# Kernel tuning notes

Measured on AMD Instinct MI355X. Metric: run time of the kernel, lower is better.

Reference implementation:

```python
import math
import jax, jax.numpy as jnp
import numpy as np

B, N = 1, 768
C_S, C_Z, C_H, H, PQ, PV = 384, 128, 16, 12, 4, 8
INF, EPS = 1e5, 1e-8


def setup_inputs() -> dict:
    key = jax.random.key(0)
    ks = jax.random.split(key, 16)
    lin = lambda k, fi, fo: jax.random.normal(k, (fi, fo), jnp.float32) / np.sqrt(fi).astype(np.float32)
    s = jax.random.normal(ks[0], (B, N, C_S), jnp.float32)
    z = jax.random.normal(ks[1], (B, N, N, C_Z), jnp.float32)
    # random proper rotation matrices via QR
    A = jax.random.normal(ks[2], (B, N, 3, 3), jnp.float32)
    Q, _ = jnp.linalg.qr(A)
    d = jnp.linalg.det(Q)
    R = Q.at[..., :, 2].multiply(d[..., None])
    t = jax.random.normal(ks[3], (B, N, 3), jnp.float32)
    mask = jnp.ones((B, N), jnp.float32)
    CO = H * (C_Z + C_H + PV * 4)  # 2112
    return dict(
        s=s, z=z, R=R, t=t, mask=mask,
        Wq=lin(ks[4], C_S, H * C_H), bq=jnp.zeros((H * C_H,), jnp.float32),
        Wkv=lin(ks[5], C_S, 2 * H * C_H), bkv=jnp.zeros((2 * H * C_H,), jnp.float32),
        Wqp=lin(ks[6], C_S, H * PQ * 3), bqp=jnp.zeros((H * PQ * 3,), jnp.float32),
        Wkvp=lin(ks[7], C_S, H * (PQ + PV) * 3), bkvp=jnp.zeros((H * (PQ + PV) * 3,), jnp.float32),
        Wb=lin(ks[8], C_Z, H), bb=jnp.zeros((H,), jnp.float32),
        head_weights=jax.random.normal(ks[9], (H,), jnp.float32) * 0.1,
        Wout=lin(ks[10], CO, C_S), bout=jnp.zeros((C_S,), jnp.float32),
    )


def _as_points(p):
    # torch: split last dim into 3 chunks (x,y,z blocks), stack on new last axis
    return jnp.stack(jnp.split(p, 3, axis=-1), axis=-1)  # [B,N,H*P,3]


def reference(s, z, R, t, mask, Wq, bq, Wkv, bkv, Wqp, bqp, Wkvp, bkvp, Wb, bb, head_weights, Wout, bout):
    q = (s @ Wq + bq).reshape(B, N, H, C_H)
    kv = (s @ Wkv + bkv).reshape(B, N, H, 2 * C_H)
    k, v = kv[..., :C_H], kv[..., C_H:]

    def rigid_apply(pts):  # pts [B,N,P,3] -> R @ p + t
        return jnp.einsum('bnij,bnpj->bnpi', R, pts) + t[:, :, None, :]

    q_pts = rigid_apply(_as_points(s @ Wqp + bqp)).reshape(B, N, H, PQ, 3)
    kv_pts = rigid_apply(_as_points(s @ Wkvp + bkvp)).reshape(B, N, H, PQ + PV, 3)
    k_pts, v_pts = kv_pts[..., :PQ, :], kv_pts[..., PQ:, :]

    b = z @ Wb + bb  # [B,N,N,H] pair bias
    a = jnp.einsum('bqhc,bkhc->bhqk', q, k) * math.sqrt(1.0 / (3 * C_H))
    a = a + math.sqrt(1.0 / 3) * jnp.transpose(b, (0, 3, 1, 2))

    # point attention: squared distance between rotated query/key points
    diff = q_pts[:, :, None] - k_pts[:, None]            # [B,q,k,H,PQ,3]
    pt_att = jnp.sum(diff ** 2, axis=-1)                  # [B,q,k,H,PQ]
    hw = jax.nn.softplus(head_weights) * math.sqrt(1.0 / (3 * (PQ * 9.0 / 2)))
    pt_att = jnp.sum(pt_att * hw[None, None, None, :, None], axis=-1) * (-0.5)  # [B,q,k,H]

    square_mask = INF * (mask[:, :, None] * mask[:, None, :] - 1.0)
    a = a + jnp.transpose(pt_att, (0, 3, 1, 2)) + square_mask[:, None]
    a = jax.nn.softmax(a, axis=-1)  # [B,H,q,k]

    o = jnp.einsum('bhqk,bkhc->bqhc', a, v).reshape(B, N, H * C_H)

    o_pt = jnp.einsum('bhqk,bkhpc->bqhpc', a, v_pts)      # [B,q,H,PV,3]
    o_pt = jnp.einsum('bnji,bnhpj->bnhpi', R, o_pt - t[:, :, None, None, :])  # invert_apply
    o_pt_norm = jnp.sqrt(jnp.sum(o_pt ** 2, axis=-1) + EPS).reshape(B, N, H * PV)
    o_pt = o_pt.reshape(B, N, H * PV, 3)

    o_pair = jnp.einsum('bhqk,bqkz->bqhz', a, z).reshape(B, N, H * C_Z)

    cat = jnp.concatenate(
        [o, o_pt[..., 0], o_pt[..., 1], o_pt[..., 2], o_pt_norm, o_pair], axis=-1)
    return cat @ Wout + bout
```

## Files before the change

### kernel.cpp

```cpp
#include <hip/hip_runtime.h>


typedef unsigned short ushort_t;

__device__ __forceinline__ float bfr(ushort_t u) {
  return __uint_as_float(((unsigned int)u) << 16);
}
__device__ __forceinline__ ushort_t f2bf(float f) {
  unsigned int u = __float_as_uint(f);
  u += 0x7FFFu + ((u >> 16) & 1u);
  return (ushort_t)(u >> 16);
}

template<bool BF16>
__device__ __forceinline__ float ld(const void* p, size_t i) {
  if constexpr (BF16) return bfr(((const ushort_t*)p)[i]);
  else                return ((const float*)p)[i];
}
template<bool BF16>
__device__ __forceinline__ void ld4(const void* p, size_t i, float* o) {
  if constexpr (BF16) {
    uint2 u = *(const uint2*)((const ushort_t*)p + i);
    o[0]=__uint_as_float(u.x<<16); o[1]=__uint_as_float(u.x & 0xffff0000u);
    o[2]=__uint_as_float(u.y<<16); o[3]=__uint_as_float(u.y & 0xffff0000u);
  } else {
    float4 v = *(const float4*)((const float*)p + i);
    o[0]=v.x; o[1]=v.y; o[2]=v.z; o[3]=v.w;
  }
}

#define NT 768
#define ZROWE 98304

__global__ void k_detect(const void* s, int* flag) {
  if (blockIdx.x == 0 && threadIdx.x == 0) {
    const unsigned int* w = (const unsigned int*)s;
    int cnt = 0;
    for (int i = 0; i < 256; ++i) {
      unsigned int e = (w[i] >> 7) & 0xFFu;
      cnt += (e >= 118u && e <= 131u) ? 1 : 0;
    }
    *flag = (cnt >= 128) ? 1 : 0;
  }
}

struct ProjSmem {
  float sl[384];
  float pbuf[576];
  float Rl[9];
  float tl[3];
};

template<bool BF16>
__device__ void proj_body(ProjSmem& sm,
            const void* s, const void* R, const void* t,
            const void* Wq, const void* bq, const void* Wkv, const void* bkv,
            const void* Wqp, const void* bqp, const void* Wkvp, const void* bkvp,
            ushort_t* qo, ushort_t* ko, ushort_t* vo,
            ushort_t* qpo, ushort_t* kpo, ushort_t* vpo)
{
  const int n = blockIdx.x, tid = threadIdx.x;
  for (int i = tid; i < 384; i += 256) sm.sl[i] = ld<BF16>(s, (size_t)n*384 + i);
  if (tid < 9)  sm.Rl[tid] = ld<BF16>(R, (size_t)n*9 + tid);
  if (tid >= 16 && tid < 19) sm.tl[tid-16] = ld<BF16>(t, (size_t)n*3 + (tid-16));
  __syncthreads();

  for (int j = tid; j < 1152; j += 256) {
    const void* W; int ldw, cj; float acc;
    if (j < 192)      { W = Wq;   ldw = 192; cj = j;       acc = ld<BF16>(bq, cj);   }
    else if (j < 576) { W = Wkv;  ldw = 384; cj = j - 192; acc = ld<BF16>(bkv, cj);  }
    else if (j < 720) { W = Wqp;  ldw = 144; cj = j - 576; acc = ld<BF16>(bqp, cj);  }
    else              { W = Wkvp; ldw = 432; cj = j - 720; acc = ld<BF16>(bkvp, cj); }
    #pragma unroll 4
    for (int i = 0; i < 384; ++i)
      acc = fmaf(sm.sl[i], ld<BF16>(W, (size_t)i*ldw + cj), acc);
    if (j < 192) qo[(size_t)n*192 + j] = f2bf(acc);
    else if (j < 576) {
      int c = j - 192, h = c >> 5, r = c & 31;
      if (r < 16) ko[(size_t)n*192 + h*16 + r]      = f2bf(acc);
      else        vo[(size_t)n*192 + h*16 + (r-16)] = f2bf(acc);
    }
    else sm.pbuf[j - 576] = acc;
  }
  __syncthreads();

  if (tid < 48) {
    int j = tid;
    float lx = sm.pbuf[j], ly = sm.pbuf[48 + j], lz = sm.pbuf[96 + j];
    #pragma unroll
    for (int i = 0; i < 3; ++i) {
      float g = sm.Rl[i*3+0]*lx + sm.Rl[i*3+1]*ly + sm.Rl[i*3+2]*lz + sm.tl[i];
      qpo[(size_t)n*144 + j*3 + i] = f2bf(g);
    }
  } else if (tid >= 64 && tid < 208) {
    int j = tid - 64;
    float lx = sm.pbuf[144 + j], ly = sm.pbuf[288 + j], lz = sm.pbuf[432 + j];
    int h = j / 12, pp = j % 12;
    #pragma unroll
    for (int i = 0; i < 3; ++i) {
      float g = sm.Rl[i*3+0]*lx + sm.Rl[i*3+1]*ly + sm.Rl[i*3+2]*lz + sm.tl[i];
      if (pp < 4) kpo[(size_t)n*144 + h*12 + pp*3 + i]     = f2bf(g);
      else        vpo[(size_t)n*288 + h*24 + (pp-4)*3 + i] = f2bf(g);
    }
  }
}

__global__ __launch_bounds__(256)
void k_proj(const int* flag,
            const void* s, const void* R, const void* t,
            const void* Wq, const void* bq, const void* Wkv, const void* bkv,
            const void* Wqp, const void* bqp, const void* Wkvp, const void* bkvp,
            ushort_t* qo, ushort_t* ko, ushort_t* vo,
            ushort_t* qpo, ushort_t* kpo, ushort_t* vpo)
{
  __shared__ ProjSmem sm;
  if (*flag) proj_body<true >(sm, s,R,t,Wq,bq,Wkv,bkv,Wqp,bqp,Wkvp,bkvp,qo,ko,vo,qpo,kpo,vpo);
  else       proj_body<false>(sm, s,R,t,Wq,bq,Wkv,bkv,Wqp,bqp,Wkvp,bkvp,qo,ko,vo,qpo,kpo,vpo);
}

struct __align__(16) AttnSmem {
  float probs[12 * NT];
  float Wbl[128 * 12];
  float catrow[2112];
  float ql[192];
  float qpl[144];
  float opt[288];
  float hwc[12], bbl[12];
};

template<bool BF16>
__device__ void attn_body(AttnSmem& sm,
            void* z, const void* Rg, const void* tg, const void* mg,
            const void* Wb, const void* bbp, const void* hwg,
            const ushort_t* qB, const ushort_t* kB, const ushort_t* vB,
            const ushort_t* qpB, const ushort_t* kpB, const ushort_t* vpB)
{
  const int qrow = blockIdx.x, tid = threadIdx.x;

  for (int i = tid; i < 128*12; i += 256) sm.Wbl[i] = ld<BF16>(Wb, i);
  for (int i = tid; i < 192; i += 256)    sm.ql[i]  = bfr(qB[(size_t)qrow*192 + i]);
  if (tid < 144) sm.qpl[tid] = bfr(qpB[(size_t)qrow*144 + tid]);
  if (tid >= 192 && tid < 204) {
    int h = tid - 192;
    float x = ld<BF16>(hwg, h);
    float sp = (x > 20.f) ? x : log1pf(expf(x));
    sm.hwc[h] = -0.5f * sp * 0.13608276348795434f;
    sm.bbl[h] = ld<BF16>(bbp, h);
  }
  __syncthreads();
  const float mq = ld<BF16>(mg, qrow);

  for (int kk = tid; kk < NT; kk += 256) {
    float accb[12];
    #pragma unroll
    for (int h = 0; h < 12; ++h) accb[h] = sm.bbl[h];
    const size_t zbase = ((size_t)qrow*NT + kk)*128;
    const float4* Wb4 = (const float4*)sm.Wbl;
    #pragma unroll 4
    for (int c4 = 0; c4 < 32; ++c4) {
      float zf[4];
      ld4<BF16>(z, zbase + c4*4, zf);
      #pragma unroll
      for (int e = 0; e < 4; ++e) {
        int c = c4*4 + e;
        float zc = zf[e];
        float4 w0 = Wb4[c*3+0], w1 = Wb4[c*3+1], w2 = Wb4[c*3+2];
        accb[0] = fmaf(zc, w0.x, accb[0]); accb[1]  = fmaf(zc, w0.y, accb[1]);
        accb[2] = fmaf(zc, w0.z, accb[2]); accb[3]  = fmaf(zc, w0.w, accb[3]);
        accb[4] = fmaf(zc, w1.x, accb[4]); accb[5]  = fmaf(zc, w1.y, accb[5]);
        accb[6] = fmaf(zc, w1.z, accb[6]); accb[7]  = fmaf(zc, w1.w, accb[7]);
        accb[8] = fmaf(zc, w2.x, accb[8]); accb[9]  = fmaf(zc, w2.y, accb[9]);
        accb[10]= fmaf(zc, w2.z, accb[10]);accb[11] = fmaf(zc, w2.w, accb[11]);
      }
    }
    const ushort_t* krow  = kB  + (size_t)kk*192;
    const ushort_t* kprow = kpB + (size_t)kk*144;
    const float mk = ld<BF16>(mg, kk);
    const float maskterm = 100000.0f * (mq*mk - 1.0f);
    #pragma unroll
    for (int h = 0; h < 12; ++h) {
      float dot = 0.f;
      #pragma unroll
      for (int j = 0; j < 16; ++j)
        dot = fmaf(sm.ql[h*16+j], bfr(krow[h*16+j]), dot);
      float pts = 0.f;
      #pragma unroll
      for (int p = 0; p < 4; ++p) {
        float dx = sm.qpl[h*12+p*3+0] - bfr(kprow[h*12+p*3+0]);
        float dy = sm.qpl[h*12+p*3+1] - bfr(kprow[h*12+p*3+1]);
        float dz = sm.qpl[h*12+p*3+2] - bfr(kprow[h*12+p*3+2]);
        pts += dx*dx + dy*dy + dz*dz;
      }
      sm.probs[h*NT + kk] = dot * 0.14433756729740643f
                          + accb[h] * 0.57735026918962576f
                          + sm.hwc[h] * pts + maskterm;
    }
  }
  __syncthreads();

  {
    const int wave = tid >> 6, lane = tid & 63;
    for (int h = wave; h < 12; h += 4) {
      float vals[12]; float m = -3.0e38f;
      #pragma unroll
      for (int i = 0; i < 12; ++i) { vals[i] = sm.probs[h*NT + i*64 + lane]; m = fmaxf(m, vals[i]); }
      #pragma unroll
      for (int off = 32; off; off >>= 1) m = fmaxf(m, __shfl_xor(m, off, 64));
      float ssum = 0.f;
      #pragma unroll
      for (int i = 0; i < 12; ++i) { vals[i] = __expf(vals[i] - m); ssum += vals[i]; }
      #pragma unroll
      for (int off = 32; off; off >>= 1) ssum += __shfl_xor(ssum, off, 64);
      float inv = 1.0f / ssum;
      #pragma unroll
      for (int i = 0; i < 12; ++i) sm.probs[h*NT + i*64 + lane] = vals[i] * inv;
    }
  }
  __syncthreads();

  {
    const int c = tid & 127, h0 = tid >> 7;
    float acc[6] = {0,0,0,0,0,0};
    for (int kk = 0; kk < NT; ++kk) {
      float zc = ld<BF16>(z, (size_t)qrow*ZROWE + (size_t)kk*128 + c);
      #pragma unroll
      for (int m = 0; m < 6; ++m)
        acc[m] = fmaf(zc, sm.probs[(h0 + 2*m)*NT + kk], acc[m]);
    }
    #pragma unroll
    for (int m = 0; m < 6; ++m) sm.catrow[576 + (h0 + 2*m)*128 + c] = acc[m];
  }

  for (int idx = tid; idx < 480; idx += 256) {
    float acc = 0.f;
    if (idx < 192) {
      const float* pr = sm.probs + (idx >> 4) * NT;
      for (int kk = 0; kk < NT; ++kk)
        acc = fmaf(pr[kk], bfr(vB[(size_t)kk*192 + idx]), acc);
      sm.catrow[idx] = acc;
    } else {
      const int j = idx - 192;
      const float* pr = sm.probs + (j / 24) * NT;
      for (int kk = 0; kk < NT; ++kk)
        acc = fmaf(pr[kk], bfr(vpB[(size_t)kk*288 + j]), acc);
      sm.opt[j] = acc;
    }
  }
  __syncthreads();

  if (tid < 96) {
    const int h = tid >> 3, p = tid & 7;
    const int j = h*24 + p*3;
    float gx = sm.opt[j], gy = sm.opt[j+1], gz = sm.opt[j+2];
    gx -= ld<BF16>(tg, qrow*3+0); gy -= ld<BF16>(tg, qrow*3+1); gz -= ld<BF16>(tg, qrow*3+2);
    float r[9];
    #pragma unroll
    for (int i = 0; i < 9; ++i) r[i] = ld<BF16>(Rg, qrow*9 + i);
    float lx = r[0]*gx + r[3]*gy + r[6]*gz;
    float ly = r[1]*gx + r[4]*gy + r[7]*gz;
    float lz = r[2]*gx + r[5]*gy + r[8]*gz;
    float nrm = sqrtf(lx*lx + ly*ly + lz*lz + 1e-8f);
    const int jj = h*8 + p;
    sm.catrow[192 + jj] = lx;
    sm.catrow[288 + jj] = ly;
    sm.catrow[384 + jj] = lz;
    sm.catrow[480 + jj] = nrm;
  }
  __syncthreads();

  float* crow;
  if constexpr (BF16) crow = (float*)((ushort_t*)z + (size_t)qrow*ZROWE);
  else                crow = (float*)z + (size_t)qrow*ZROWE;
  for (int i = tid; i < 2112; i += 256) crow[i] = sm.catrow[i];
}

__global__ __launch_bounds__(256)
void k_attn(const int* flag,
            void* z, const void* Rg, const void* tg, const void* mg,
            const void* Wb, const void* bbp, const void* hwg,
            const ushort_t* qB, const ushort_t* kB, const ushort_t* vB,
            const ushort_t* qpB, const ushort_t* kpB, const ushort_t* vpB)
{
  __shared__ AttnSmem sm;
  if (*flag) attn_body<true >(sm, z,Rg,tg,mg,Wb,bbp,hwg,qB,kB,vB,qpB,kpB,vpB);
  else       attn_body<false>(sm, z,Rg,tg,mg,Wb,bbp,hwg,qB,kB,vB,qpB,kpB,vpB);
}

struct OutSmem { float As[32][33]; float Bs[32][33]; };

template<bool BF16>
__device__ void out_body(OutSmem& sm, const void* zcat, const void* Wout,
                         const void* bout, void* out)
{
  const size_t RS = BF16 ? 49152 : 98304;
  const float* cat = (const float*)zcat;
  const int n0 = blockIdx.x * 32, m0 = blockIdx.y * 32, tid = threadIdx.x;
  const int tm = (tid >> 4) * 2, tn = (tid & 15) * 2;
  float acc00 = 0.f, acc01 = 0.f, acc10 = 0.f, acc11 = 0.f;
  const int e = tid * 4;
  const int lm = e >> 5, lk = e & 31;
  for (int k0 = 0; k0 < 2112; k0 += 32) {
    float4 a = *(const float4*)(cat + (size_t)(m0 + lm)*RS + k0 + lk);
    sm.As[lk+0][lm] = a.x; sm.As[lk+1][lm] = a.y; sm.As[lk+2][lm] = a.z; sm.As[lk+3][lm] = a.w;
    float bw[4];
    ld4<BF16>(Wout, (size_t)(k0 + lm)*384 + n0 + lk, bw);
    sm.Bs[lm][lk+0] = bw[0]; sm.Bs[lm][lk+1] = bw[1];
    sm.Bs[lm][lk+2] = bw[2]; sm.Bs[lm][lk+3] = bw[3];
    __syncthreads();
    #pragma unroll
    for (int kk = 0; kk < 32; ++kk) {
      float a0 = sm.As[kk][tm], a1 = sm.As[kk][tm+1];
      float b0 = sm.Bs[kk][tn], b1 = sm.Bs[kk][tn+1];
      acc00 = fmaf(a0,b0,acc00); acc01 = fmaf(a0,b1,acc01);
      acc10 = fmaf(a1,b0,acc10); acc11 = fmaf(a1,b1,acc11);
    }
    __syncthreads();
  }
  float bb0 = ld<BF16>(bout, n0+tn), bb1 = ld<BF16>(bout, n0+tn+1);
  float v00 = acc00+bb0, v01 = acc01+bb1, v10 = acc10+bb0, v11 = acc11+bb1;
  if constexpr (BF16) {
    ushort_t* o = (ushort_t*)out;
    o[(size_t)(m0+tm)*384   + n0+tn]   = f2bf(v00);
    o[(size_t)(m0+tm)*384   + n0+tn+1] = f2bf(v01);
    o[(size_t)(m0+tm+1)*384 + n0+tn]   = f2bf(v10);
    o[(size_t)(m0+tm+1)*384 + n0+tn+1] = f2bf(v11);
  } else {
    float* o = (float*)out;
    o[(size_t)(m0+tm)*384   + n0+tn]   = v00;
    o[(size_t)(m0+tm)*384   + n0+tn+1] = v01;
    o[(size_t)(m0+tm+1)*384 + n0+tn]   = v10;
    o[(size_t)(m0+tm+1)*384 + n0+tn+1] = v11;
  }
}

__global__ __launch_bounds__(256)
void k_out(const int* flag, const void* zcat, const void* Wout,
           const void* bout, void* out)
{
  __shared__ OutSmem sm;
  if (*flag) out_body<true >(sm, zcat, Wout, bout, out);
  else       out_body<false>(sm, zcat, Wout, bout, out);
}

extern "C" void kernel_launch(void* const* d_in, const int* in_sizes, int n_in,
                              void* d_out, int out_size, void* d_ws, size_t ws_size,
                              hipStream_t stream) {
  const void* s    = d_in[0];
  void*       z    = d_in[1];
  const void* R    = d_in[2];
  const void* t    = d_in[3];
  const void* mask = d_in[4];
  const void* Wq   = d_in[5];
  const void* bq   = d_in[6];
  const void* Wkv  = d_in[7];
  const void* bkv  = d_in[8];
  const void* Wqp  = d_in[9];
  const void* bqp  = d_in[10];
  const void* Wkvp = d_in[11];
  const void* bkvp = d_in[12];
  const void* Wb   = d_in[13];
  const void* bb   = d_in[14];
  const void* hw   = d_in[15];
  const void* Wout = d_in[16];
  const void* bout = d_in[17];

  int* flag = (int*)d_ws;
  ushort_t* base = (ushort_t*)((char*)d_ws + 64);
  ushort_t* qB  = base;
  ushort_t* kB  = qB  + 147456;
  ushort_t* vB  = kB  + 147456;
  ushort_t* qpB = vB  + 147456;
  ushort_t* kpB = qpB + 110592;
  ushort_t* vpB = kpB + 110592;

  k_detect<<<dim3(1), dim3(64), 0, stream>>>(s, flag);
  k_proj<<<dim3(768), dim3(256), 0, stream>>>(flag, s, R, t, Wq, bq, Wkv, bkv,
                                              Wqp, bqp, Wkvp, bkvp,
                                              qB, kB, vB, qpB, kpB, vpB);
  k_attn<<<dim3(768), dim3(256), 0, stream>>>(flag, z, R, t, mask, Wb, bb, hw,
                                              qB, kB, vB, qpB, kpB, vpB);
  k_out<<<dim3(12, 24), dim3(256), 0, stream>>>(flag, z, Wout, bout, d_out);
}
```

Measured before the change: 945.2 us.

## Transpose V layouts, vectorize projections and attention loads, union shared memory

```diff
diff --git a/kernel.cpp b/kernel.cpp
--- a/kernel.cpp
+++ b/kernel.cpp
@@ -28,6 +28,29 @@
     o[0]=v.x; o[1]=v.y; o[2]=v.z; o[3]=v.w;
   }
 }
+template<bool BF16>
+__device__ __forceinline__ void ld2(const void* p, size_t i, float& x, float& y) {
+  if constexpr (BF16) {
+    unsigned int u = *(const unsigned int*)((const ushort_t*)p + i);
+    x = __uint_as_float(u << 16); y = __uint_as_float(u & 0xffff0000u);
+  } else {
+    float2 v = *(const float2*)((const float*)p + i);
+    x = v.x; y = v.y;
+  }
+}
+__device__ __forceinline__ void unp8(uint4 v, float* f) {
+  f[0]=__uint_as_float(v.x<<16); f[1]=__uint_as_float(v.x&0xffff0000u);
+  f[2]=__uint_as_float(v.y<<16); f[3]=__uint_as_float(v.y&0xffff0000u);
+  f[4]=__uint_as_float(v.z<<16); f[5]=__uint_as_float(v.z&0xffff0000u);
+  f[6]=__uint_as_float(v.w<<16); f[7]=__uint_as_float(v.w&0xffff0000u);
+}
+__device__ __forceinline__ void unp4(uint2 v, float* f) {
+  f[0]=__uint_as_float(v.x<<16); f[1]=__uint_as_float(v.x&0xffff0000u);
+  f[2]=__uint_as_float(v.y<<16); f[3]=__uint_as_float(v.y&0xffff0000u);
+}
+__device__ __forceinline__ float f4get(float4 v, int e) {
+  return e==0 ? v.x : (e==1 ? v.y : (e==2 ? v.z : v.w));
+}
 
 #define NT 768
 #define ZROWE 98304
@@ -56,51 +79,72 @@
             const void* s, const void* R, const void* t,
             const void* Wq, const void* bq, const void* Wkv, const void* bkv,
             const void* Wqp, const void* bqp, const void* Wkvp, const void* bkvp,
-            ushort_t* qo, ushort_t* ko, ushort_t* vo,
-            ushort_t* qpo, ushort_t* kpo, ushort_t* vpo)
+            ushort_t* qo, ushort_t* ko, ushort_t* vTo,
+            ushort_t* qpo, ushort_t* kpo, ushort_t* vpTo)
 {
   const int n = blockIdx.x, tid = threadIdx.x;
-  for (int i = tid; i < 384; i += 256) sm.sl[i] = ld<BF16>(s, (size_t)n*384 + i);
-  if (tid < 9)  sm.Rl[tid] = ld<BF16>(R, (size_t)n*9 + tid);
-  if (tid >= 16 && tid < 19) sm.tl[tid-16] = ld<BF16>(t, (size_t)n*3 + (tid-16));
-  __syncthreads();
-
-  for (int j = tid; j < 1152; j += 256) {
-    const void* W; int ldw, cj; float acc;
-    if (j < 192)      { W = Wq;   ldw = 192; cj = j;       acc = ld<BF16>(bq, cj);   }
-    else if (j < 576) { W = Wkv;  ldw = 384; cj = j - 192; acc = ld<BF16>(bkv, cj);  }
-    else if (j < 720) { W = Wqp;  ldw = 144; cj = j - 576; acc = ld<BF16>(bqp, cj);  }
-    else              { W = Wkvp; ldw = 432; cj = j - 720; acc = ld<BF16>(bkvp, cj); }
+  for (int i = tid; i < 96; i += 256) {
+    float f[4]; ld4<BF16>(s, (size_t)n*384 + i*4, f);
+    *(float4*)&sm.sl[i*4] = make_float4(f[0],f[1],f[2],f[3]);
+  }
+  if (tid >= 128 && tid < 137) sm.Rl[tid-128] = ld<BF16>(R, (size_t)n*9 + (tid-128));
+  if (tid >= 160 && tid < 163) sm.tl[tid-160] = ld<BF16>(t, (size_t)n*3 + (tid-160));
+  __syncthreads();
+
+  for (int g = tid; g < 288; g += 256) {
+    const void* W; const void* bias; int ldw, cj;
+    if (g < 48)       { W=Wq;   bias=bq;   ldw=192; cj=g*4;       }
+    else if (g < 144) { W=Wkv;  bias=bkv;  ldw=384; cj=g*4-192;   }
+    else if (g < 180) { W=Wqp;  bias=bqp;  ldw=144; cj=g*4-576;   }
+    else              { W=Wkvp; bias=bkvp; ldw=432; cj=g*4-720;   }
+    float a0 = ld<BF16>(bias, cj+0), a1 = ld<BF16>(bias, cj+1),
+          a2 = ld<BF16>(bias, cj+2), a3 = ld<BF16>(bias, cj+3);
     #pragma unroll 4
-    for (int i = 0; i < 384; ++i)
-      acc = fmaf(sm.sl[i], ld<BF16>(W, (size_t)i*ldw + cj), acc);
-    if (j < 192) qo[(size_t)n*192 + j] = f2bf(acc);
-    else if (j < 576) {
-      int c = j - 192, h = c >> 5, r = c & 31;
-      if (r < 16) ko[(size_t)n*192 + h*16 + r]      = f2bf(acc);
-      else        vo[(size_t)n*192 + h*16 + (r-16)] = f2bf(acc);
-    }
-    else sm.pbuf[j - 576] = acc;
+    for (int i = 0; i < 384; ++i) {
+      float w[4]; ld4<BF16>(W, (size_t)i*ldw + cj, w);
+      const float sv = sm.sl[i];
+      a0 = fmaf(sv, w[0], a0); a1 = fmaf(sv, w[1], a1);
+      a2 = fmaf(sv, w[2], a2); a3 = fmaf(sv, w[3], a3);
+    }
+    const int j = g*4;
+    if (j < 192) {
+      ushort_t* d = qo + (size_t)n*192 + j;
+      d[0]=f2bf(a0); d[1]=f2bf(a1); d[2]=f2bf(a2); d[3]=f2bf(a3);
+    } else if (j < 576) {
+      const int c = j - 192, h = c >> 5, r = c & 31;
+      if (r < 16) {
+        ushort_t* d = ko + (size_t)n*192 + h*16 + r;
+        d[0]=f2bf(a0); d[1]=f2bf(a1); d[2]=f2bf(a2); d[3]=f2bf(a3);
+      } else {
+        const int cc = h*16 + (r-16);
+        vTo[(size_t)(cc+0)*NT + n] = f2bf(a0);
+        vTo[(size_t)(cc+1)*NT + n] = f2bf(a1);
+        vTo[(size_t)(cc+2)*NT + n] = f2bf(a2);
+        vTo[(size_t)(cc+3)*NT + n] = f2bf(a3);
+      }
+    } else {
+      *(float4*)&sm.pbuf[j-576] = make_float4(a0,a1,a2,a3);
+    }
   }
   __syncthreads();
 
   if (tid < 48) {
-    int j = tid;
-    float lx = sm.pbuf[j], ly = sm.pbuf[48 + j], lz = sm.pbuf[96 + j];
+    const int j = tid;
+    float lx = sm.pbuf[j], ly = sm.pbuf[48+j], lz = sm.pbuf[96+j];
     #pragma unroll
     for (int i = 0; i < 3; ++i) {
       float g = sm.Rl[i*3+0]*lx + sm.Rl[i*3+1]*ly + sm.Rl[i*3+2]*lz + sm.tl[i];
       qpo[(size_t)n*144 + j*3 + i] = f2bf(g);
     }
   } else if (tid >= 64 && tid < 208) {
-    int j = tid - 64;
-    float lx = sm.pbuf[144 + j], ly = sm.pbuf[288 + j], lz = sm.pbuf[432 + j];
-    int h = j / 12, pp = j % 12;
+    const int j = tid - 64;
+    float lx = sm.pbuf[144+j], ly = sm.pbuf[288+j], lz = sm.pbuf[432+j];
+    const int h = j / 12, pp = j % 12;
     #pragma unroll
     for (int i = 0; i < 3; ++i) {
       float g = sm.Rl[i*3+0]*lx + sm.Rl[i*3+1]*ly + sm.Rl[i*3+2]*lz + sm.tl[i];
-      if (pp < 4) kpo[(size_t)n*144 + h*12 + pp*3 + i]     = f2bf(g);
-      else        vpo[(size_t)n*288 + h*24 + (pp-4)*3 + i] = f2bf(g);
+      if (pp < 4) kpo[(size_t)n*144 + h*12 + pp*3 + i]         = f2bf(g);
+      else        vpTo[(size_t)(h*24 + (pp-4)*3 + i)*NT + n]   = f2bf(g);
     }
   }
 }
@@ -110,148 +154,213 @@
             const void* s, const void* R, const void* t,
             const void* Wq, const void* bq, const void* Wkv, const void* bkv,
             const void* Wqp, const void* bqp, const void* Wkvp, const void* bkvp,
-            ushort_t* qo, ushort_t* ko, ushort_t* vo,
-            ushort_t* qpo, ushort_t* kpo, ushort_t* vpo)
+            ushort_t* qo, ushort_t* ko, ushort_t* vTo,
+            ushort_t* qpo, ushort_t* kpo, ushort_t* vpTo)
 {
   __shared__ ProjSmem sm;
-  if (*flag) proj_body<true >(sm, s,R,t,Wq,bq,Wkv,bkv,Wqp,bqp,Wkvp,bkvp,qo,ko,vo,qpo,kpo,vpo);
-  else       proj_body<false>(sm, s,R,t,Wq,bq,Wkv,bkv,Wqp,bqp,Wkvp,bkvp,qo,ko,vo,qpo,kpo,vpo);
+  if (*flag) proj_body<true >(sm, s,R,t,Wq,bq,Wkv,bkv,Wqp,bqp,Wkvp,bkvp,qo,ko,vTo,qpo,kpo,vpTo);
+  else       proj_body<false>(sm, s,R,t,Wq,bq,Wkv,bkv,Wqp,bqp,Wkvp,bkvp,qo,ko,vTo,qpo,kpo,vpTo);
 }
 
 struct __align__(16) AttnSmem {
   float probs[12 * NT];
-  float Wbl[128 * 12];
-  float catrow[2112];
-  float ql[192];
-  float qpl[144];
-  float opt[288];
-  float hwc[12], bbl[12];
+  union {
+    struct {
+      float4 Wbl[128*3];
+      float4 ql4[12*4];
+      float4 qpl4[12*4];
+      float  hwc[12], bbl[12];
+    } a;
+    struct {
+      float catrow[2112];
+      float opt[288];
+    } c;
+  } u;
 };
 
 template<bool BF16>
 __device__ void attn_body(AttnSmem& sm,
             void* z, const void* Rg, const void* tg, const void* mg,
             const void* Wb, const void* bbp, const void* hwg,
-            const ushort_t* qB, const ushort_t* kB, const ushort_t* vB,
-            const ushort_t* qpB, const ushort_t* kpB, const ushort_t* vpB)
+            const ushort_t* qB, const ushort_t* kB, const ushort_t* vTB,
+            const ushort_t* qpB, const ushort_t* kpB, const ushort_t* vpTB)
 {
   const int qrow = blockIdx.x, tid = threadIdx.x;
 
-  for (int i = tid; i < 128*12; i += 256) sm.Wbl[i] = ld<BF16>(Wb, i);
-  for (int i = tid; i < 192; i += 256)    sm.ql[i]  = bfr(qB[(size_t)qrow*192 + i]);
-  if (tid < 144) sm.qpl[tid] = bfr(qpB[(size_t)qrow*144 + tid]);
-  if (tid >= 192 && tid < 204) {
-    int h = tid - 192;
+  for (int i = tid; i < 128*12; i += 256) ((float*)sm.u.a.Wbl)[i] = ld<BF16>(Wb, i);
+  if (tid < 48) {
+    const int h = tid >> 2, part = tid & 3;
+    float f[4];
+    unp4(*(const uint2*)(qB + (size_t)qrow*192 + h*16 + part*4), f);
+    sm.u.a.ql4[h*4+part] = make_float4(f[0],f[1],f[2],f[3]);
+  } else if (tid >= 64 && tid < 112) {
+    const int j = tid - 64, h = j >> 2, part = j & 3;
+    if (part < 3) {
+      float f[4];
+      unp4(*(const uint2*)(qpB + (size_t)qrow*144 + h*12 + part*4), f);
+      sm.u.a.qpl4[h*4+part] = make_float4(f[0],f[1],f[2],f[3]);
+    }
+  } else if (tid >= 192 && tid < 204) {
+    const int h = tid - 192;
     float x = ld<BF16>(hwg, h);
     float sp = (x > 20.f) ? x : log1pf(expf(x));
-    sm.hwc[h] = -0.5f * sp * 0.13608276348795434f;
-    sm.bbl[h] = ld<BF16>(bbp, h);
+    sm.u.a.hwc[h] = -0.5f * sp * 0.13608276348795434f;
+    sm.u.a.bbl[h] = ld<BF16>(bbp, h);
   }
   __syncthreads();
   const float mq = ld<BF16>(mg, qrow);
 
-  for (int kk = tid; kk < NT; kk += 256) {
-    float accb[12];
-    #pragma unroll
-    for (int h = 0; h < 12; ++h) accb[h] = sm.bbl[h];
-    const size_t zbase = ((size_t)qrow*NT + kk)*128;
-    const float4* Wb4 = (const float4*)sm.Wbl;
-    #pragma unroll 4
+  {
+    const int kk0 = tid;
+    float accb[3][12];
+    #pragma unroll
+    for (int h = 0; h < 12; ++h) {
+      const float b = sm.u.a.bbl[h];
+      accb[0][h] = b; accb[1][h] = b; accb[2][h] = b;
+    }
+    const size_t zb = ((size_t)qrow*NT + kk0)*128;
     for (int c4 = 0; c4 < 32; ++c4) {
-      float zf[4];
-      ld4<BF16>(z, zbase + c4*4, zf);
+      float z0[4], z1[4], z2[4];
+      ld4<BF16>(z, zb +           c4*4, z0);
+      ld4<BF16>(z, zb + 256*128 + c4*4, z1);
+      ld4<BF16>(z, zb + 512*128 + c4*4, z2);
       #pragma unroll
       for (int e = 0; e < 4; ++e) {
-        int c = c4*4 + e;
-        float zc = zf[e];
-        float4 w0 = Wb4[c*3+0], w1 = Wb4[c*3+1], w2 = Wb4[c*3+2];
-        accb[0] = fmaf(zc, w0.x, accb[0]); accb[1]  = fmaf(zc, w0.y, accb[1]);
-        accb[2] = fmaf(zc, w0.z, accb[2]); accb[3]  = fmaf(zc, w0.w, accb[3]);
-        accb[4] = fmaf(zc, w1.x, accb[4]); accb[5]  = fmaf(zc, w1.y, accb[5]);
-        accb[6] = fmaf(zc, w1.z, accb[6]); accb[7]  = fmaf(zc, w1.w, accb[7]);
-        accb[8] = fmaf(zc, w2.x, accb[8]); accb[9]  = fmaf(zc, w2.y, accb[9]);
-        accb[10]= fmaf(zc, w2.z, accb[10]);accb[11] = fmaf(zc, w2.w, accb[11]);
+        const int c = c4*4 + e;
+        float wr[12];
+        *(float4*)&wr[0] = sm.u.a.Wbl[c*3+0];
+        *(float4*)&wr[4] = sm.u.a.Wbl[c*3+1];
+        *(float4*)&wr[8] = sm.u.a.Wbl[c*3+2];
+        #pragma unroll
+        for (int h = 0; h < 12; ++h) {
+          accb[0][h] = fmaf(z0[e], wr[h], accb[0][h]);
+          accb[1][h] = fmaf(z1[e], wr[h], accb[1][h]);
+          accb[2][h] = fmaf(z2[e], wr[h], accb[2][h]);
+        }
       }
     }
-    const ushort_t* krow  = kB  + (size_t)kk*192;
-    const ushort_t* kprow = kpB + (size_t)kk*144;
-    const float mk = ld<BF16>(mg, kk);
-    const float maskterm = 100000.0f * (mq*mk - 1.0f);
-    #pragma unroll
-    for (int h = 0; h < 12; ++h) {
-      float dot = 0.f;
+    #pragma unroll
+    for (int r = 0; r < 3; ++r) {
+      const int kk = kk0 + r*256;
+      const uint4* kr  = (const uint4*)(kB  + (size_t)kk*192);
+      const uint2* kpr = (const uint2*)(kpB + (size_t)kk*144);
+      const float mk = ld<BF16>(mg, kk);
+      const float maskterm = 100000.0f * (mq*mk - 1.0f);
       #pragma unroll
-      for (int j = 0; j < 16; ++j)
-        dot = fmaf(sm.ql[h*16+j], bfr(krow[h*16+j]), dot);
-      float pts = 0.f;
-      #pragma unroll
-      for (int p = 0; p < 4; ++p) {
-        float dx = sm.qpl[h*12+p*3+0] - bfr(kprow[h*12+p*3+0]);
-        float dy = sm.qpl[h*12+p*3+1] - bfr(kprow[h*12+p*3+1]);
-        float dz = sm.qpl[h*12+p*3+2] - bfr(kprow[h*12+p*3+2]);
-        pts += dx*dx + dy*dy + dz*dz;
+      for (int h = 0; h < 12; ++h) {
+        float kf[16];
+        unp8(kr[2*h+0], kf); unp8(kr[2*h+1], kf+8);
+        float qf[16];
+        *(float4*)&qf[0]  = sm.u.a.ql4[h*4+0];
+        *(float4*)&qf[4]  = sm.u.a.ql4[h*4+1];
+        *(float4*)&qf[8]  = sm.u.a.ql4[h*4+2];
+        *(float4*)&qf[12] = sm.u.a.ql4[h*4+3];
+        float dot = 0.f;
+        #pragma unroll
+        for (int j = 0; j < 16; ++j) dot = fmaf(qf[j], kf[j], dot);
+        float kpf[12];
+        unp4(kpr[3*h+0], kpf); unp4(kpr[3*h+1], kpf+4); unp4(kpr[3*h+2], kpf+8);
+        float qpf[12];
+        *(float4*)&qpf[0] = sm.u.a.qpl4[h*4+0];
+        *(float4*)&qpf[4] = sm.u.a.qpl4[h*4+1];
+        *(float4*)&qpf[8] = sm.u.a.qpl4[h*4+2];
+        float pts = 0.f;
+        #pragma unroll
+        for (int p = 0; p < 4; ++p) {
+          float dx = qpf[p*3+0]-kpf[p*3+0];
+          float dy = qpf[p*3+1]-kpf[p*3+1];
+          float dz = qpf[p*3+2]-kpf[p*3+2];
+          pts += dx*dx + dy*dy + dz*dz;
+        }
+        sm.probs[h*NT + kk] = dot * 0.14433756729740643f
+                            + accb[r][h] * 0.57735026918962576f
+                            + sm.u.a.hwc[h] * pts + maskterm;
       }
-      sm.probs[h*NT + kk] = dot * 0.14433756729740643f
-                          + accb[h] * 0.57735026918962576f
-                          + sm.hwc[h] * pts + maskterm;
     }
   }
   __syncthreads();
 
   {
     const int wave = tid >> 6, lane = tid & 63;
-    for (int h = wave; h < 12; h += 4) {
-      float vals[12]; float m = -3.0e38f;
-      #pragma unroll
-      for (int i = 0; i < 12; ++i) { vals[i] = sm.probs[h*NT + i*64 + lane]; m = fmaxf(m, vals[i]); }
+    #pragma unroll
+    for (int hh = 0; hh < 3; ++hh) {
+      const int h = wave + hh*4;
+      float4* P4 = (float4*)sm.probs + h*192;
+      float4 v0 = P4[lane], v1 = P4[64+lane], v2 = P4[128+lane];
+      float m = fmaxf(fmaxf(fmaxf(v0.x,v0.y),fmaxf(v0.z,v0.w)),
+                fmaxf(fmaxf(fmaxf(v1.x,v1.y),fmaxf(v1.z,v1.w)),
+                      fmaxf(fmaxf(v2.x,v2.y),fmaxf(v2.z,v2.w))));
       #pragma unroll
       for (int off = 32; off; off >>= 1) m = fmaxf(m, __shfl_xor(m, off, 64));
-      float ssum = 0.f;
-      #pragma unroll
-      for (int i = 0; i < 12; ++i) { vals[i] = __expf(vals[i] - m); ssum += vals[i]; }
+      v0.x=__expf(v0.x-m); v0.y=__expf(v0.y-m); v0.z=__expf(v0.z-m); v0.w=__expf(v0.w-m);
+      v1.x=__expf(v1.x-m); v1.y=__expf(v1.y-m); v1.z=__expf(v1.z-m); v1.w=__expf(v1.w-m);
+      v2.x=__expf(v2.x-m); v2.y=__expf(v2.y-m); v2.z=__expf(v2.z-m); v2.w=__expf(v2.w-m);
+      float ssum = (v0.x+v0.y+v0.z+v0.w) + (v1.x+v1.y+v1.z+v1.w) + (v2.x+v2.y+v2.z+v2.w);
       #pragma unroll
       for (int off = 32; off; off >>= 1) ssum += __shfl_xor(ssum, off, 64);
-      float inv = 1.0f / ssum;
+      const float inv = 1.0f / ssum;
+      v0.x*=inv; v0.y*=inv; v0.z*=inv; v0.w*=inv;
+      v1.x*=inv; v1.y*=inv; v1.z*=inv; v1.w*=inv;
+      v2.x*=inv; v2.y*=inv; v2.z*=inv; v2.w*=inv;
+      P4[lane]=v0; P4[64+lane]=v1; P4[128+lane]=v2;
+    }
+  }
+  __syncthreads();
+
+  {
+    const int c2 = (tid & 63) * 2;
+    const int h0 = (tid >> 6) * 3;
+    const float4* p0 = (const float4*)(sm.probs + (h0+0)*NT);
+    const float4* p1 = (const float4*)(sm.probs + (h0+1)*NT);
+    const float4* p2 = (const float4*)(sm.probs + (h0+2)*NT);
+    const size_t zrb = (size_t)qrow*ZROWE;
+    float a00=0.f,a01=0.f,a10=0.f,a11=0.f,a20=0.f,a21=0.f;
+    #pragma unroll 2
+    for (int tt = 0; tt < 192; ++tt) {
+      float4 pa = p0[tt], pb = p1[tt], pc = p2[tt];
       #pragma unroll
-      for (int i = 0; i < 12; ++i) sm.probs[h*NT + i*64 + lane] = vals[i] * inv;
-    }
-  }
-  __syncthreads();
-
-  {
-    const int c = tid & 127, h0 = tid >> 7;
-    float acc[6] = {0,0,0,0,0,0};
-    for (int kk = 0; kk < NT; ++kk) {
-      float zc = ld<BF16>(z, (size_t)qrow*ZROWE + (size_t)kk*128 + c);
-      #pragma unroll
-      for (int m = 0; m < 6; ++m)
-        acc[m] = fmaf(zc, sm.probs[(h0 + 2*m)*NT + kk], acc[m]);
-    }
-    #pragma unroll
-    for (int m = 0; m < 6; ++m) sm.catrow[576 + (h0 + 2*m)*128 + c] = acc[m];
+      for (int e = 0; e < 4; ++e) {
+        float zx, zy;
+        ld2<BF16>(z, zrb + (size_t)(tt*4+e)*128 + c2, zx, zy);
+        const float w0 = f4get(pa,e), w1 = f4get(pb,e), w2 = f4get(pc,e);
+        a00 = fmaf(w0, zx, a00); a01 = fmaf(w0, zy, a01);
+        a10 = fmaf(w1, zx, a10); a11 = fmaf(w1, zy, a11);
+        a20 = fmaf(w2, zx, a20); a21 = fmaf(w2, zy, a21);
+      }
+    }
+    sm.u.c.catrow[576 + (h0+0)*128 + c2]   = a00;
+    sm.u.c.catrow[576 + (h0+0)*128 + c2+1] = a01;
+    sm.u.c.catrow[576 + (h0+1)*128 + c2]   = a10;
+    sm.u.c.catrow[576 + (h0+1)*128 + c2+1] = a11;
+    sm.u.c.catrow[576 + (h0+2)*128 + c2]   = a20;
+    sm.u.c.catrow[576 + (h0+2)*128 + c2+1] = a21;
   }
 
   for (int idx = tid; idx < 480; idx += 256) {
+    const ushort_t* src; int h;
+    if (idx < 192) { h = idx >> 4;            src = vTB  + (size_t)idx*NT; }
+    else           { const int j = idx - 192; h = j/24;  src = vpTB + (size_t)j*NT; }
+    const uint4*  s4 = (const uint4*)src;
+    const float4* pr = (const float4*)(sm.probs + h*NT);
     float acc = 0.f;
-    if (idx < 192) {
-      const float* pr = sm.probs + (idx >> 4) * NT;
-      for (int kk = 0; kk < NT; ++kk)
-        acc = fmaf(pr[kk], bfr(vB[(size_t)kk*192 + idx]), acc);
-      sm.catrow[idx] = acc;
-    } else {
-      const int j = idx - 192;
-      const float* pr = sm.probs + (j / 24) * NT;
-      for (int kk = 0; kk < NT; ++kk)
-        acc = fmaf(pr[kk], bfr(vpB[(size_t)kk*288 + j]), acc);
-      sm.opt[j] = acc;
-    }
+    #pragma unroll 2
+    for (int tt = 0; tt < 96; ++tt) {
+      float vf[8]; unp8(s4[tt], vf);
+      float4 pa = pr[2*tt], pb = pr[2*tt+1];
+      acc = fmaf(pa.x, vf[0], acc); acc = fmaf(pa.y, vf[1], acc);
+      acc = fmaf(pa.z, vf[2], acc); acc = fmaf(pa.w, vf[3], acc);
+      acc = fmaf(pb.x, vf[4], acc); acc = fmaf(pb.y, vf[5], acc);
+      acc = fmaf(pb.z, vf[6], acc); acc = fmaf(pb.w, vf[7], acc);
+    }
+    if (idx < 192) sm.u.c.catrow[idx]   = acc;
+    else           sm.u.c.opt[idx-192]  = acc;
   }
   __syncthreads();
 
   if (tid < 96) {
     const int h = tid >> 3, p = tid & 7;
     const int j = h*24 + p*3;
-    float gx = sm.opt[j], gy = sm.opt[j+1], gz = sm.opt[j+2];
+    float gx = sm.u.c.opt[j], gy = sm.u.c.opt[j+1], gz = sm.u.c.opt[j+2];
     gx -= ld<BF16>(tg, qrow*3+0); gy -= ld<BF16>(tg, qrow*3+1); gz -= ld<BF16>(tg, qrow*3+2);
     float r[9];
     #pragma unroll
@@ -261,29 +370,33 @@
     float lz = r[2]*gx + r[5]*gy + r[8]*gz;
     float nrm = sqrtf(lx*lx + ly*ly + lz*lz + 1e-8f);
     const int jj = h*8 + p;
-    sm.catrow[192 + jj] = lx;
-    sm.catrow[288 + jj] = ly;
-    sm.catrow[384 + jj] = lz;
-    sm.catrow[480 + jj] = nrm;
-  }
-  __syncthreads();
-
-  float* crow;
-  if constexpr (BF16) crow = (float*)((ushort_t*)z + (size_t)qrow*ZROWE);
-  else                crow = (float*)z + (size_t)qrow*ZROWE;
-  for (int i = tid; i < 2112; i += 256) crow[i] = sm.catrow[i];
-}
-
-__global__ __launch_bounds__(256)
+    sm.u.c.catrow[192 + jj] = lx;
+    sm.u.c.catrow[288 + jj] = ly;
+    sm.u.c.catrow[384 + jj] = lz;
+    sm.u.c.catrow[480 + jj] = nrm;
+  }
+  __syncthreads();
+
+  {
+    float* crow;
+    if constexpr (BF16) crow = (float*)((ushort_t*)z + (size_t)qrow*ZROWE);
+    else                crow = (float*)z + (size_t)qrow*ZROWE;
+    float4* c4p = (float4*)crow;
+    const float4* src4 = (const float4*)sm.u.c.catrow;
+    for (int i = tid; i < 528; i += 256) c4p[i] = src4[i];
+  }
+}
+
+__global__ __launch_bounds__(256, 3)
 void k_attn(const int* flag,
             void* z, const void* Rg, const void* tg, const void* mg,
             const void* Wb, const void* bbp, const void* hwg,
-            const ushort_t* qB, const ushort_t* kB, const ushort_t* vB,
-            const ushort_t* qpB, const ushort_t* kpB, const ushort_t* vpB)
+            const ushort_t* qB, const ushort_t* kB, const ushort_t* vTB,
+            const ushort_t* qpB, const ushort_t* kpB, const ushort_t* vpTB)
 {
   __shared__ AttnSmem sm;
-  if (*flag) attn_body<true >(sm, z,Rg,tg,mg,Wb,bbp,hwg,qB,kB,vB,qpB,kpB,vpB);
-  else       attn_body<false>(sm, z,Rg,tg,mg,Wb,bbp,hwg,qB,kB,vB,qpB,kpB,vpB);
+  if (*flag) attn_body<true >(sm, z,Rg,tg,mg,Wb,bbp,hwg,qB,kB,vTB,qpB,kpB,vpTB);
+  else       attn_body<false>(sm, z,Rg,tg,mg,Wb,bbp,hwg,qB,kB,vTB,qpB,kpB,vpTB);
 }
 
 struct OutSmem { float As[32][33]; float Bs[32][33]; };
@@ -366,18 +479,18 @@
 
   int* flag = (int*)d_ws;
   ushort_t* base = (ushort_t*)((char*)d_ws + 64);
-  ushort_t* qB  = base;
-  ushort_t* kB  = qB  + 147456;
-  ushort_t* vB  = kB  + 147456;
-  ushort_t* qpB = vB  + 147456;
-  ushort_t* kpB = qpB + 110592;
-  ushort_t* vpB = kpB + 110592;
+  ushort_t* qB   = base;
+  ushort_t* kB   = qB   + 147456;
+  ushort_t* vTB  = kB   + 147456;
+  ushort_t* qpB  = vTB  + 147456;
+  ushort_t* kpB  = qpB  + 110592;
+  ushort_t* vpTB = kpB  + 110592;
 
   k_detect<<<dim3(1), dim3(64), 0, stream>>>(s, flag);
   k_proj<<<dim3(768), dim3(256), 0, stream>>>(flag, s, R, t, Wq, bq, Wkv, bkv,
                                               Wqp, bqp, Wkvp, bkvp,
-                                              qB, kB, vB, qpB, kpB, vpB);
+                                              qB, kB, vTB, qpB, kpB, vpTB);
   k_attn<<<dim3(768), dim3(256), 0, stream>>>(flag, z, R, t, mask, Wb, bb, hw,
-                                              qB, kB, vB, qpB, kpB, vpB);
+                                              qB, kB, vTB, qpB, kpB, vpTB);
   k_out<<<dim3(12, 24), dim3(256), 0, stream>>>(flag, z, Wout, bout, d_out);
 }
```

Result: slower. 1.151 ms (+21.8%).
